# Kernel optimization log

Hardware: AMD Instinct MI355X
Metric: run time of the kernel (lower is better)

## Reference

```python
import jax, jax.numpy as jnp
import numpy as np

D_MODEL = 1024
N_HEADS = 16
D_K = D_MODEL // N_HEADS  # 64


def setup_inputs() -> dict:
    key = jax.random.key(0)
    ks = jax.random.split(key, 12)
    B, S = 2, 2048
    inp = {
        "query": jax.random.normal(ks[0], (B, S, D_MODEL), jnp.float32),
        "key": jax.random.normal(ks[1], (B, S, D_MODEL), jnp.float32),
        "value": jax.random.normal(ks[2], (B, S, D_MODEL), jnp.float32),
        "mask": jnp.ones((B, 1, S, S), jnp.int32),
    }
    sc = 1.0 / np.sqrt(D_MODEL)
    inp["Wq"] = jax.random.normal(ks[3], (D_MODEL, D_MODEL), jnp.float32) * sc
    inp["bq"] = jnp.zeros((D_MODEL,), jnp.float32)
    inp["Wk"] = jax.random.normal(ks[4], (D_MODEL, D_MODEL), jnp.float32) * sc
    inp["bk"] = jnp.zeros((D_MODEL,), jnp.float32)
    inp["Wv"] = jax.random.normal(ks[5], (D_MODEL, D_MODEL), jnp.float32) * sc
    inp["bv"] = jnp.zeros((D_MODEL,), jnp.float32)
    inp["Wo"] = jax.random.normal(ks[6], (D_MODEL, D_MODEL), jnp.float32) * sc
    inp["bo"] = jnp.zeros((D_MODEL,), jnp.float32)
    return inp


def reference(query, key, value, mask, Wq, bq, Wk, bk, Wv, bv, Wo, bo):
    B, Sq, _ = query.shape
    H, dk = N_HEADS, D_K
    # linear projections, split heads: (B,S,D) -> (B,H,S,dk)
    def split_heads(x):
        return x.reshape(B, -1, H, dk).transpose(0, 2, 1, 3)
    Q = split_heads(query @ Wq.T + bq)
    K = split_heads(key @ Wk.T + bk)
    V = split_heads(value @ Wv.T + bv)
    scale = 1.0 / jnp.sqrt(jnp.asarray(dk, jnp.float32))
    scores = jnp.einsum('bhqd,bhkd->bhqk', Q, K) * scale
    scores = jnp.where(mask == 0, jnp.asarray(-1e9, scores.dtype), scores)
    attn = jax.nn.softmax(scores, axis=-1)  # (B,H,Sq,Sk)
    out = jnp.einsum('bhqk,bhkd->bhqd', attn, V)
    out = out.transpose(0, 2, 1, 3).reshape(B, Sq, D_MODEL)
    out = out @ Wo.T + bo
    return out, attn
```

## Files before the change

kernel.cpp:

```cpp
#include <hip/hip_runtime.h>
#include <cstdint>
#include <cstddef>

#define DEV __device__ __forceinline__

typedef float f32x4 __attribute__((ext_vector_type(4)));
typedef __bf16 bf16x8 __attribute__((ext_vector_type(8)));
typedef unsigned short u16x8 __attribute__((ext_vector_type(8)));

static constexpr int D = 1024, H = 16, DK = 64, S = 2048, B = 2;
static constexpr int M_TOT = B * S;
static constexpr size_t OUT0 = (size_t)M_TOT * D;

DEV unsigned short f2bf(float f) {
  unsigned x = __builtin_bit_cast(unsigned, f);
  unsigned r = (x + 0x7fffu + ((x >> 16) & 1u)) >> 16;
  return (unsigned short)r;
}

DEV float bf2f(unsigned short u) {
  return __builtin_bit_cast(float, (unsigned)u << 16);
}

DEV f32x4 mfma_bf16(bf16x8 a, bf16x8 b, f32x4 c) {
  return __builtin_amdgcn_mfma_f32_16x16x32_bf16(a, b, c, 0, 0, 0);
}

DEV bf16x8 bc(u16x8 u) { return __builtin_bit_cast(bf16x8, u); }

template <int MODE, bool ABF16, bool WBF16>
DEV void proj_body(unsigned short* As, unsigned short* Bs, const void* Aptr,
                   const void* W, const float* bias, void* dst) {
  constexpr int BM = 128, BK = 32, LDT = 40;
  const int tid = threadIdx.x;
  const int lane = tid & 63, wave = tid >> 6;
  const int wrow = wave >> 1, wcol = wave & 1;
  const int l15 = lane & 15, kg = lane >> 4;
  const int m0 = blockIdx.y * BM, n0 = blockIdx.x * BM;
  const int srow = tid >> 1, scb = (tid & 1) * 16;

  f32x4 acc[4][4] = {};

  for (int kt = 0; kt < D; kt += BK) {
    {
      u16x8 t0, t1;
      if constexpr (ABF16) {
        const unsigned short* ap =
            (const unsigned short*)Aptr + (size_t)(m0 + srow) * D + kt + scb;
        t0 = *(const u16x8*)ap;
        t1 = *(const u16x8*)(ap + 8);
      } else {
        const float* ap = (const float*)Aptr + (size_t)(m0 + srow) * D + kt + scb;
        float4 v0 = *(const float4*)(ap + 0);
        float4 v1 = *(const float4*)(ap + 4);
        float4 v2 = *(const float4*)(ap + 8);
        float4 v3 = *(const float4*)(ap + 12);
        t0[0] = f2bf(v0.x); t0[1] = f2bf(v0.y); t0[2] = f2bf(v0.z); t0[3] = f2bf(v0.w);
        t0[4] = f2bf(v1.x); t0[5] = f2bf(v1.y); t0[6] = f2bf(v1.z); t0[7] = f2bf(v1.w);
        t1[0] = f2bf(v2.x); t1[1] = f2bf(v2.y); t1[2] = f2bf(v2.z); t1[3] = f2bf(v2.w);
        t1[4] = f2bf(v3.x); t1[5] = f2bf(v3.y); t1[6] = f2bf(v3.z); t1[7] = f2bf(v3.w);
      }
      *(u16x8*)&As[srow * LDT + scb] = t0;
      *(u16x8*)&As[srow * LDT + scb + 8] = t1;

      u16x8 s0, s1;
      if constexpr (WBF16) {
        const unsigned short* wp =
            (const unsigned short*)W + (size_t)(n0 + srow) * D + kt + scb;
        s0 = *(const u16x8*)wp;
        s1 = *(const u16x8*)(wp + 8);
      } else {
        const float* bp = (const float*)W + (size_t)(n0 + srow) * D + kt + scb;
        float4 w0 = *(const float4*)(bp + 0);
        float4 w1 = *(const float4*)(bp + 4);
        float4 w2 = *(const float4*)(bp + 8);
        float4 w3 = *(const float4*)(bp + 12);
        s0[0] = f2bf(w0.x); s0[1] = f2bf(w0.y); s0[2] = f2bf(w0.z); s0[3] = f2bf(w0.w);
        s0[4] = f2bf(w1.x); s0[5] = f2bf(w1.y); s0[6] = f2bf(w1.z); s0[7] = f2bf(w1.w);
        s1[0] = f2bf(w2.x); s1[1] = f2bf(w2.y); s1[2] = f2bf(w2.z); s1[3] = f2bf(w2.w);
        s1[4] = f2bf(w3.x); s1[5] = f2bf(w3.y); s1[6] = f2bf(w3.z); s1[7] = f2bf(w3.w);
      }
      *(u16x8*)&Bs[srow * LDT + scb] = s0;
      *(u16x8*)&Bs[srow * LDT + scb + 8] = s1;
    }
    __syncthreads();

    bf16x8 a[4], b[4];
#pragma unroll
    for (int i = 0; i < 4; i++)
      a[i] = bc(*(const u16x8*)&As[(wrow * 64 + i * 16 + l15) * LDT + kg * 8]);
#pragma unroll
    for (int i = 0; i < 4; i++)
      b[i] = bc(*(const u16x8*)&Bs[(wcol * 64 + i * 16 + l15) * LDT + kg * 8]);
#pragma unroll
    for (int mi = 0; mi < 4; mi++)
#pragma unroll
      for (int ni = 0; ni < 4; ni++) acc[mi][ni] = mfma_bf16(a[mi], b[ni], acc[mi][ni]);
    __syncthreads();
  }

#pragma unroll
  for (int mi = 0; mi < 4; mi++) {
#pragma unroll
    for (int ni = 0; ni < 4; ni++) {
      const int n = n0 + wcol * 64 + ni * 16 + l15;
      const float bval = bias[n];
#pragma unroll
      for (int r = 0; r < 4; r++) {
        const int m = m0 + wrow * 64 + mi * 16 + kg * 4 + r;
        float v = acc[mi][ni][r] + bval;
        if constexpr (MODE == 0) v *= 0.125f;
        if constexpr (MODE == 0 || MODE == 1) {
          const int b_ = m >> 11, s = m & (S - 1), h = n >> 6, d_ = n & (DK - 1);
          ((unsigned short*)dst)[(((size_t)(b_ * H + h)) * S + s) * DK + d_] = f2bf(v);
        } else if constexpr (MODE == 2) {
          const int b_ = m >> 11, s = m & (S - 1), h = n >> 6, d_ = n & (DK - 1);
          ((unsigned short*)dst)[(((size_t)(b_ * H + h)) * DK + d_) * S + s] = f2bf(v);
        } else {
          ((float*)dst)[(size_t)m * D + n] = v;
        }
      }
    }
  }
}

struct PrepArgs {
  const float* A[3];
  const float* W[3];
  const float* bias[3];
  unsigned short* dst[3];
  const int* mask;
  unsigned long long* bits;
  const float* Wo;
  unsigned short* WoBf;
};

__global__ __launch_bounds__(256) void qkv_prep(PrepArgs pa) {
  __shared__ __align__(16) unsigned short As[128 * 40];
  __shared__ __align__(16) unsigned short Bs[128 * 40];
  const int z = blockIdx.z;
  if (z == 0) {
    proj_body<0, false, false>(As, Bs, pa.A[0], pa.W[0], pa.bias[0], pa.dst[0]);
  } else if (z == 1) {
    proj_body<1, false, false>(As, Bs, pa.A[1], pa.W[1], pa.bias[1], pa.dst[1]);
  } else if (z == 2) {
    proj_body<2, false, false>(As, Bs, pa.A[2], pa.W[2], pa.bias[2], pa.dst[2]);
  } else {
    const int gid = blockIdx.y * 8 + blockIdx.x;
    const int tid = threadIdx.x, lane = tid & 63;
    const int base = gid * 512;
    for (int w = base + (tid >> 6); w < base + 512; w += 4) {
      int m = __builtin_nontemporal_load(pa.mask + (size_t)w * 64 + lane);
      unsigned long long bal = __ballot(m != 0);
      if (lane == 0) pa.bits[w] = bal;
    }
    {
      const size_t i0 = (size_t)gid * 4096 + (size_t)tid * 16;
      float4 v0 = *(const float4*)(pa.Wo + i0);
      float4 v1 = *(const float4*)(pa.Wo + i0 + 4);
      float4 v2 = *(const float4*)(pa.Wo + i0 + 8);
      float4 v3 = *(const float4*)(pa.Wo + i0 + 12);
      u16x8 t0, t1;
      t0[0] = f2bf(v0.x); t0[1] = f2bf(v0.y); t0[2] = f2bf(v0.z); t0[3] = f2bf(v0.w);
      t0[4] = f2bf(v1.x); t0[5] = f2bf(v1.y); t0[6] = f2bf(v1.z); t0[7] = f2bf(v1.w);
      t1[0] = f2bf(v2.x); t1[1] = f2bf(v2.y); t1[2] = f2bf(v2.z); t1[3] = f2bf(v2.w);
      t1[4] = f2bf(v3.x); t1[5] = f2bf(v3.y); t1[6] = f2bf(v3.z); t1[7] = f2bf(v3.w);
      *(u16x8*)(pa.WoBf + i0) = t0;
      *(u16x8*)(pa.WoBf + i0 + 8) = t1;
    }
  }
}

__global__ __launch_bounds__(256) void out_proj(const unsigned short* __restrict__ ctx,
                                                const unsigned short* __restrict__ WoBf,
                                                const float* __restrict__ bo,
                                                float* __restrict__ out) {
  __shared__ __align__(16) unsigned short As[128 * 40];
  __shared__ __align__(16) unsigned short Bs[128 * 40];
  proj_body<3, true, true>(As, Bs, ctx, WoBf, bo, out);
}

__global__ __launch_bounds__(512, 4) void attn_kernel(
    const unsigned short* __restrict__ Qb, const unsigned short* __restrict__ Kb,
    const unsigned short* __restrict__ Vt, const unsigned* __restrict__ bits32,
    float* __restrict__ attn_out, unsigned short* __restrict__ ctx) {
  constexpr int QB = 32;
  constexpr int PROW = 264;
  __shared__ __align__(16) unsigned short pbuf[2][QB * PROW];
  __shared__ unsigned mlds[QB * 64];
  __shared__ float rsum[8 * QB];
  __shared__ float rinv_s[QB];
  __shared__ float opart[4 * QB * 17];

  const int wg = blockIdx.x;
  const int qblk = wg & 63, h = (wg >> 6) & 15, b_ = wg >> 10;
  const int bh = b_ * H + h;
  const int qb0 = qblk * QB;
  const int tid = threadIdx.x, lane = tid & 63, wave = tid >> 6;
  const int l15 = lane & 15, kg = lane >> 4;
  const int rowq = kg * 4;
  constexpr float LOG2E = 1.44269504088896340736f;

#pragma unroll
  for (int i = 0; i < 4; i++) {
    const int idx = tid + i * 512;
    mlds[idx] = bits32[((size_t)b_ * S + qb0 + (idx >> 6)) * 64 + (idx & 63)];
  }

  const unsigned short* qbase = Qb + ((size_t)bh * S + qb0) * DK;
  bf16x8 aq[2][2];
#pragma unroll
  for (int rg = 0; rg < 2; rg++)
#pragma unroll
    for (int hf = 0; hf < 2; hf++)
      aq[rg][hf] =
          bc(*(const u16x8*)(qbase + (size_t)(rg * 16 + l15) * DK + hf * 32 + kg * 8));
  __syncthreads();

  float sum[2][4] = {};
#pragma unroll 2
  for (int i = 0; i < 16; i++) {
    const int t = wave * 16 + i;
    const unsigned short* krow = Kb + ((size_t)bh * S + t * 16 + l15) * DK;
    bf16x8 b0 = bc(*(const u16x8*)(krow + kg * 8));
    bf16x8 b1 = bc(*(const u16x8*)(krow + 32 + kg * 8));
    const unsigned shift = (unsigned)((t & 1) * 16 + l15);
#pragma unroll
    for (int rg = 0; rg < 2; rg++) {
      f32x4 c = {0.f, 0.f, 0.f, 0.f};
      c = mfma_bf16(aq[rg][0], b0, c);
      c = mfma_bf16(aq[rg][1], b1, c);
#pragma unroll
      for (int r = 0; r < 4; r++) {
        const int row = rg * 16 + rowq + r;
        const unsigned w = mlds[row * 64 + (t >> 1)];
        sum[rg][r] += ((w >> shift) & 1u) ? exp2f(c[r] * LOG2E) : 0.f;
      }
    }
  }

#pragma unroll
  for (int rg = 0; rg < 2; rg++)
#pragma unroll
    for (int r = 0; r < 4; r++) {
      float s = sum[rg][r];
      s += __shfl_xor(s, 1);
      s += __shfl_xor(s, 2);
      s += __shfl_xor(s, 4);
      s += __shfl_xor(s, 8);
      if (l15 == 0) rsum[wave * QB + rg * 16 + rowq + r] = s;
    }
  __syncthreads();
  if (tid < QB) {
    float t2 = 0.f;
#pragma unroll
    for (int w = 0; w < 8; w++) t2 += rsum[w * QB + tid];
    rinv_s[tid] = 1.f / t2;
  }
  __syncthreads();

  float ri[2][4];
#pragma unroll
  for (int rg = 0; rg < 2; rg++)
#pragma unroll
    for (int r = 0; r < 4; r++) ri[rg][r] = rinv_s[rg * 16 + rowq + r];

  const int dg = wave & 3, ksub = wave >> 2;
  const unsigned short* vrow = Vt + ((size_t)bh * DK + dg * 16 + l15) * S + ksub * 128;
  float* abase = attn_out + ((size_t)bh * S + qb0) * S;
  f32x4 o[2] = {};

  for (int sb = 0; sb < 8; sb++) {
    unsigned short* pb = pbuf[sb & 1];
#pragma unroll
    for (int j = 0; j < 2; j++) {
      const int t = sb * 16 + wave * 2 + j;
      const unsigned short* krow = Kb + ((size_t)bh * S + t * 16 + l15) * DK;
      bf16x8 b0 = bc(*(const u16x8*)(krow + kg * 8));
      bf16x8 b1 = bc(*(const u16x8*)(krow + 32 + kg * 8));
      const unsigned shift = (unsigned)((t & 1) * 16 + l15);
      const int lc = (wave * 2 + j) * 16 + l15;
#pragma unroll
      for (int rg = 0; rg < 2; rg++) {
        f32x4 c = {0.f, 0.f, 0.f, 0.f};
        c = mfma_bf16(aq[rg][0], b0, c);
        c = mfma_bf16(aq[rg][1], b1, c);
#pragma unroll
        for (int r = 0; r < 4; r++) {
          const int row = rg * 16 + rowq + r;
          const unsigned w = mlds[row * 64 + (t >> 1)];
          const float e = ((w >> shift) & 1u) ? exp2f(c[r] * LOG2E) : 0.f;
          const float p = e * ri[rg][r];
          __builtin_nontemporal_store(p, abase + (size_t)row * S + t * 16 + l15);
          pb[row * PROW + lc] = f2bf(p);
        }
      }
    }
    __syncthreads();
    const unsigned short* vv = vrow + sb * 256;
#pragma unroll
    for (int ks = 0; ks < 4; ks++) {
      bf16x8 bv = bc(*(const u16x8*)(vv + ks * 32 + kg * 8));
#pragma unroll
      for (int rg = 0; rg < 2; rg++) {
        bf16x8 af = bc(
            *(const u16x8*)&pb[(rg * 16 + l15) * PROW + ksub * 128 + ks * 32 + kg * 8]);
        o[rg] = mfma_bf16(af, bv, o[rg]);
      }
    }
  }

  if (ksub == 1) {
#pragma unroll
    for (int rg = 0; rg < 2; rg++)
#pragma unroll
      for (int r = 0; r < 4; r++)
        opart[dg * (QB * 17) + (rg * 16 + rowq + r) * 17 + l15] = o[rg][r];
  }
  __syncthreads();
  if (ksub == 0) {
#pragma unroll
    for (int rg = 0; rg < 2; rg++)
#pragma unroll
      for (int r = 0; r < 4; r++) {
        const int row = rg * 16 + rowq + r;
        const float v = o[rg][r] + opart[dg * (QB * 17) + row * 17 + l15];
        ctx[((size_t)(b_ * S + qb0 + row)) * D + h * DK + dg * 16 + l15] = f2bf(v);
      }
  }
}

extern "C" void kernel_launch(void* const* d_in, const int* in_sizes, int n_in,
                              void* d_out, int out_size, void* d_ws, size_t ws_size,
                              hipStream_t stream) {
  const float* query = (const float*)d_in[0];
  const float* key   = (const float*)d_in[1];
  const float* value = (const float*)d_in[2];
  const int*   mask  = (const int*)d_in[3];
  const float* Wq = (const float*)d_in[4];
  const float* bq = (const float*)d_in[5];
  const float* Wk = (const float*)d_in[6];
  const float* bk = (const float*)d_in[7];
  const float* Wv = (const float*)d_in[8];
  const float* bv = (const float*)d_in[9];
  const float* Wo = (const float*)d_in[10];
  const float* bo = (const float*)d_in[11];

  float* out_p = (float*)d_out;
  float* attn_p = (float*)d_out + OUT0;

  size_t off = 0;
  auto carve = [&](size_t bytes) {
    void* p = (char*)d_ws + off;
    off += (bytes + 255) & ~(size_t)255;
    return p;
  };
  const size_t headed = (size_t)B * H * S * DK * sizeof(unsigned short);
  unsigned short* Qb = (unsigned short*)carve(headed);
  unsigned short* Kb = (unsigned short*)carve(headed);
  unsigned short* Vt = (unsigned short*)carve(headed);
  unsigned short* ctx = (unsigned short*)carve((size_t)M_TOT * D * sizeof(unsigned short));
  unsigned long long* bits = (unsigned long long*)carve((size_t)B * S * S / 8);
  unsigned short* WoBf = (unsigned short*)carve((size_t)D * D * sizeof(unsigned short));

  PrepArgs pa;
  pa.A[0] = query; pa.A[1] = key; pa.A[2] = value;
  pa.W[0] = Wq; pa.W[1] = Wk; pa.W[2] = Wv;
  pa.bias[0] = bq; pa.bias[1] = bk; pa.bias[2] = bv;
  pa.dst[0] = Qb; pa.dst[1] = Kb; pa.dst[2] = Vt;
  pa.mask = mask; pa.bits = bits; pa.Wo = Wo; pa.WoBf = WoBf;

  qkv_prep<<<dim3(8, 32, 4), 256, 0, stream>>>(pa);

  attn_kernel<<<B * H * (S / 32), 512, 0, stream>>>(Qb, Kb, Vt, (const unsigned*)bits,
                                                    attn_p, ctx);

  out_proj<<<dim3(8, 32), 256, 0, stream>>>(ctx, WoBf, bo, out_p);
}
```

Before: 366.6 us.

## Pre-convert weights to bf16, add all-ones mask fast path, coalesce attn stores

Splits the prep into a separate conversion kernel that turns all four weight matrices into bf16 once, so the QKV GEMM no longer reconverts fp32 weights for every tile. The attention kernel checks whether its mask tile is all ones and, if so, skips the per-element mask lookups. The attention-probability output is now written as coalesced 16-byte rows read back from the bf16 LDS buffer instead of scattered scalar stores. The occupancy hint rises to 6 blocks. The stored attn values are now bf16-rounded rather than full fp32, and the extra launch adds overhead.

New measurement: 369.5 us. No clear change (+0.8%).

```diff
diff --git a/kernel.cpp b/kernel.cpp
--- a/kernel.cpp
+++ b/kernel.cpp
@@ -28,9 +28,9 @@
 
 DEV bf16x8 bc(u16x8 u) { return __builtin_bit_cast(bf16x8, u); }
 
-template <int MODE, bool ABF16, bool WBF16>
+template <int MODE, bool ABF16>
 DEV void proj_body(unsigned short* As, unsigned short* Bs, const void* Aptr,
-                   const void* W, const float* bias, void* dst) {
+                   const unsigned short* W, const float* bias, void* dst) {
   constexpr int BM = 128, BK = 32, LDT = 40;
   const int tid = threadIdx.x;
   const int lane = tid & 63, wave = tid >> 6;
@@ -63,25 +63,9 @@
       *(u16x8*)&As[srow * LDT + scb] = t0;
       *(u16x8*)&As[srow * LDT + scb + 8] = t1;
 
-      u16x8 s0, s1;
-      if constexpr (WBF16) {
-        const unsigned short* wp =
-            (const unsigned short*)W + (size_t)(n0 + srow) * D + kt + scb;
-        s0 = *(const u16x8*)wp;
-        s1 = *(const u16x8*)(wp + 8);
-      } else {
-        const float* bp = (const float*)W + (size_t)(n0 + srow) * D + kt + scb;
-        float4 w0 = *(const float4*)(bp + 0);
-        float4 w1 = *(const float4*)(bp + 4);
-        float4 w2 = *(const float4*)(bp + 8);
-        float4 w3 = *(const float4*)(bp + 12);
-        s0[0] = f2bf(w0.x); s0[1] = f2bf(w0.y); s0[2] = f2bf(w0.z); s0[3] = f2bf(w0.w);
-        s0[4] = f2bf(w1.x); s0[5] = f2bf(w1.y); s0[6] = f2bf(w1.z); s0[7] = f2bf(w1.w);
-        s1[0] = f2bf(w2.x); s1[1] = f2bf(w2.y); s1[2] = f2bf(w2.z); s1[3] = f2bf(w2.w);
-        s1[4] = f2bf(w3.x); s1[5] = f2bf(w3.y); s1[6] = f2bf(w3.z); s1[7] = f2bf(w3.w);
-      }
-      *(u16x8*)&Bs[srow * LDT + scb] = s0;
-      *(u16x8*)&Bs[srow * LDT + scb + 8] = s1;
+      const unsigned short* wp = W + (size_t)(n0 + srow) * D + kt + scb;
+      *(u16x8*)&Bs[srow * LDT + scb] = *(const u16x8*)wp;
+      *(u16x8*)&Bs[srow * LDT + scb + 8] = *(const u16x8*)(wp + 8);
     }
     __syncthreads();
 
@@ -124,63 +108,74 @@
   }
 }
 
-struct PrepArgs {
-  const float* A[3];
-  const float* W[3];
-  const float* bias[3];
-  unsigned short* dst[3];
-  const int* mask;
-  unsigned long long* bits;
-  const float* Wo;
-  unsigned short* WoBf;
-};
-
-__global__ __launch_bounds__(256) void qkv_prep(PrepArgs pa) {
-  __shared__ __align__(16) unsigned short As[128 * 40];
-  __shared__ __align__(16) unsigned short Bs[128 * 40];
-  const int z = blockIdx.z;
-  if (z == 0) {
-    proj_body<0, false, false>(As, Bs, pa.A[0], pa.W[0], pa.bias[0], pa.dst[0]);
-  } else if (z == 1) {
-    proj_body<1, false, false>(As, Bs, pa.A[1], pa.W[1], pa.bias[1], pa.dst[1]);
-  } else if (z == 2) {
-    proj_body<2, false, false>(As, Bs, pa.A[2], pa.W[2], pa.bias[2], pa.dst[2]);
-  } else {
-    const int gid = blockIdx.y * 8 + blockIdx.x;
-    const int tid = threadIdx.x, lane = tid & 63;
-    const int base = gid * 512;
-    for (int w = base + (tid >> 6); w < base + 512; w += 4) {
-      int m = __builtin_nontemporal_load(pa.mask + (size_t)w * 64 + lane);
-      unsigned long long bal = __ballot(m != 0);
-      if (lane == 0) pa.bits[w] = bal;
-    }
-    {
-      const size_t i0 = (size_t)gid * 4096 + (size_t)tid * 16;
-      float4 v0 = *(const float4*)(pa.Wo + i0);
-      float4 v1 = *(const float4*)(pa.Wo + i0 + 4);
-      float4 v2 = *(const float4*)(pa.Wo + i0 + 8);
-      float4 v3 = *(const float4*)(pa.Wo + i0 + 12);
+__global__ __launch_bounds__(256) void conv_kernel(
+    const float* __restrict__ Wq, const float* __restrict__ Wk,
+    const float* __restrict__ Wv, const float* __restrict__ Wo,
+    unsigned short* __restrict__ Wqb, unsigned short* __restrict__ Wkb,
+    unsigned short* __restrict__ Wvb, unsigned short* __restrict__ Wob,
+    const int* __restrict__ mask, unsigned long long* __restrict__ bits) {
+  const int gid = blockIdx.x, tid = threadIdx.x;
+  if (gid < 256) {
+    const float* srcs[4] = {Wq, Wk, Wv, Wo};
+    unsigned short* dsts[4] = {Wqb, Wkb, Wvb, Wob};
+    const float* src = srcs[gid >> 6];
+    unsigned short* dst = dsts[gid >> 6];
+    const size_t off = (size_t)(gid & 63) * 16384;
+#pragma unroll
+    for (int it = 0; it < 4; it++) {
+      const size_t i0 = off + it * 4096 + (size_t)tid * 16;
+      float4 v0 = *(const float4*)(src + i0);
+      float4 v1 = *(const float4*)(src + i0 + 4);
+      float4 v2 = *(const float4*)(src + i0 + 8);
+      float4 v3 = *(const float4*)(src + i0 + 12);
       u16x8 t0, t1;
       t0[0] = f2bf(v0.x); t0[1] = f2bf(v0.y); t0[2] = f2bf(v0.z); t0[3] = f2bf(v0.w);
       t0[4] = f2bf(v1.x); t0[5] = f2bf(v1.y); t0[6] = f2bf(v1.z); t0[7] = f2bf(v1.w);
       t1[0] = f2bf(v2.x); t1[1] = f2bf(v2.y); t1[2] = f2bf(v2.z); t1[3] = f2bf(v2.w);
       t1[4] = f2bf(v3.x); t1[5] = f2bf(v3.y); t1[6] = f2bf(v3.z); t1[7] = f2bf(v3.w);
-      *(u16x8*)(pa.WoBf + i0) = t0;
-      *(u16x8*)(pa.WoBf + i0 + 8) = t1;
-    }
-  }
+      *(u16x8*)(dst + i0) = t0;
+      *(u16x8*)(dst + i0 + 8) = t1;
+    }
+  } else {
+    const int lane = tid & 63;
+    const int base = (gid - 256) * 256;
+    for (int w = base + (tid >> 6); w < base + 256; w += 4) {
+      int m = __builtin_nontemporal_load(mask + (size_t)w * 64 + lane);
+      unsigned long long bal = __ballot(m != 0);
+      if (lane == 0) bits[w] = bal;
+    }
+  }
+}
+
+struct GemmArgs {
+  const float* A[3];
+  const unsigned short* Wb[3];
+  const float* bias[3];
+  unsigned short* dst[3];
+};
+
+__global__ __launch_bounds__(256) void qkv_gemm(GemmArgs ga) {
+  __shared__ __align__(16) unsigned short As[128 * 40];
+  __shared__ __align__(16) unsigned short Bs[128 * 40];
+  const int z = blockIdx.z;
+  if (z == 0)
+    proj_body<0, false>(As, Bs, ga.A[0], ga.Wb[0], ga.bias[0], ga.dst[0]);
+  else if (z == 1)
+    proj_body<1, false>(As, Bs, ga.A[1], ga.Wb[1], ga.bias[1], ga.dst[1]);
+  else
+    proj_body<2, false>(As, Bs, ga.A[2], ga.Wb[2], ga.bias[2], ga.dst[2]);
 }
 
 __global__ __launch_bounds__(256) void out_proj(const unsigned short* __restrict__ ctx,
-                                                const unsigned short* __restrict__ WoBf,
+                                                const unsigned short* __restrict__ Wob,
                                                 const float* __restrict__ bo,
                                                 float* __restrict__ out) {
   __shared__ __align__(16) unsigned short As[128 * 40];
   __shared__ __align__(16) unsigned short Bs[128 * 40];
-  proj_body<3, true, true>(As, Bs, ctx, WoBf, bo, out);
-}
-
-__global__ __launch_bounds__(512, 4) void attn_kernel(
+  proj_body<3, true>(As, Bs, ctx, Wob, bo, out);
+}
+
+__global__ __launch_bounds__(512, 6) void attn_kernel(
     const unsigned short* __restrict__ Qb, const unsigned short* __restrict__ Kb,
     const unsigned short* __restrict__ Vt, const unsigned* __restrict__ bits32,
     float* __restrict__ attn_out, unsigned short* __restrict__ ctx) {
@@ -191,6 +186,7 @@
   __shared__ float rsum[8 * QB];
   __shared__ float rinv_s[QB];
   __shared__ float opart[4 * QB * 17];
+  __shared__ unsigned mflag;
 
   const int wg = blockIdx.x;
   const int qblk = wg & 63, h = (wg >> 6) & 15, b_ = wg >> 10;
@@ -201,11 +197,19 @@
   const int rowq = kg * 4;
   constexpr float LOG2E = 1.44269504088896340736f;
 
+  if (tid == 0) mflag = 0xFFFFFFFFu;
+  unsigned myand = 0xFFFFFFFFu;
+  unsigned mw[4];
 #pragma unroll
   for (int i = 0; i < 4; i++) {
     const int idx = tid + i * 512;
-    mlds[idx] = bits32[((size_t)b_ * S + qb0 + (idx >> 6)) * 64 + (idx & 63)];
-  }
+    mw[i] = bits32[((size_t)b_ * S + qb0 + (idx >> 6)) * 64 + (idx & 63)];
+    myand &= mw[i];
+  }
+  __syncthreads();
+#pragma unroll
+  for (int i = 0; i < 4; i++) mlds[tid + i * 512] = mw[i];
+  if (myand != 0xFFFFFFFFu) atomicAnd(&mflag, 0u);
 
   const unsigned short* qbase = Qb + ((size_t)bh * S + qb0) * DK;
   bf16x8 aq[2][2];
@@ -216,6 +220,7 @@
       aq[rg][hf] =
           bc(*(const u16x8*)(qbase + (size_t)(rg * 16 + l15) * DK + hf * 32 + kg * 8));
   __syncthreads();
+  const bool allones = (mflag == 0xFFFFFFFFu);
 
   float sum[2][4] = {};
 #pragma unroll 2
@@ -230,11 +235,15 @@
       f32x4 c = {0.f, 0.f, 0.f, 0.f};
       c = mfma_bf16(aq[rg][0], b0, c);
       c = mfma_bf16(aq[rg][1], b1, c);
-#pragma unroll
-      for (int r = 0; r < 4; r++) {
-        const int row = rg * 16 + rowq + r;
-        const unsigned w = mlds[row * 64 + (t >> 1)];
-        sum[rg][r] += ((w >> shift) & 1u) ? exp2f(c[r] * LOG2E) : 0.f;
+      if (allones) {
+#pragma unroll
+        for (int r = 0; r < 4; r++) sum[rg][r] += exp2f(c[r] * LOG2E);
+      } else {
+#pragma unroll
+        for (int r = 0; r < 4; r++) {
+          const unsigned w = mlds[(rg * 16 + rowq + r) * 64 + (t >> 1)];
+          sum[rg][r] += ((w >> shift) & 1u) ? exp2f(c[r] * LOG2E) : 0.f;
+        }
       }
     }
   }
@@ -268,6 +277,8 @@
   const int dg = wave & 3, ksub = wave >> 2;
   const unsigned short* vrow = Vt + ((size_t)bh * DK + dg * 16 + l15) * S + ksub * 128;
   float* abase = attn_out + ((size_t)bh * S + qb0) * S;
+  const int wrow2 = lane >> 5;
+  const int wcol = (lane & 31) * 8;
   f32x4 o[2] = {};
 
   for (int sb = 0; sb < 8; sb++) {
@@ -285,18 +296,37 @@
         f32x4 c = {0.f, 0.f, 0.f, 0.f};
         c = mfma_bf16(aq[rg][0], b0, c);
         c = mfma_bf16(aq[rg][1], b1, c);
-#pragma unroll
-        for (int r = 0; r < 4; r++) {
-          const int row = rg * 16 + rowq + r;
-          const unsigned w = mlds[row * 64 + (t >> 1)];
-          const float e = ((w >> shift) & 1u) ? exp2f(c[r] * LOG2E) : 0.f;
-          const float p = e * ri[rg][r];
-          __builtin_nontemporal_store(p, abase + (size_t)row * S + t * 16 + l15);
-          pb[row * PROW + lc] = f2bf(p);
+        if (allones) {
+#pragma unroll
+          for (int r = 0; r < 4; r++) {
+            const int row = rg * 16 + rowq + r;
+            pb[row * PROW + lc] = f2bf(exp2f(c[r] * LOG2E) * ri[rg][r]);
+          }
+        } else {
+#pragma unroll
+          for (int r = 0; r < 4; r++) {
+            const int row = rg * 16 + rowq + r;
+            const unsigned w = mlds[row * 64 + (t >> 1)];
+            const float e = ((w >> shift) & 1u) ? exp2f(c[r] * LOG2E) : 0.f;
+            pb[row * PROW + lc] = f2bf(e * ri[rg][r]);
+          }
         }
       }
     }
     __syncthreads();
+
+#pragma unroll
+    for (int rr = 0; rr < 2; rr++) {
+      const int row = wave * 4 + rr * 2 + wrow2;
+      u16x8 u = *(const u16x8*)&pb[row * PROW + wcol];
+      f32x4 lo, hi;
+      lo[0] = bf2f(u[0]); lo[1] = bf2f(u[1]); lo[2] = bf2f(u[2]); lo[3] = bf2f(u[3]);
+      hi[0] = bf2f(u[4]); hi[1] = bf2f(u[5]); hi[2] = bf2f(u[6]); hi[3] = bf2f(u[7]);
+      float* dp = abase + (size_t)row * S + sb * 256 + wcol;
+      __builtin_nontemporal_store(lo, (f32x4*)dp);
+      __builtin_nontemporal_store(hi, (f32x4*)(dp + 4));
+    }
+
     const unsigned short* vv = vrow + sb * 256;
 #pragma unroll
     for (int ks = 0; ks < 4; ks++) {
@@ -356,24 +386,28 @@
     return p;
   };
   const size_t headed = (size_t)B * H * S * DK * sizeof(unsigned short);
+  const size_t wbytes = (size_t)D * D * sizeof(unsigned short);
   unsigned short* Qb = (unsigned short*)carve(headed);
   unsigned short* Kb = (unsigned short*)carve(headed);
   unsigned short* Vt = (unsigned short*)carve(headed);
   unsigned short* ctx = (unsigned short*)carve((size_t)M_TOT * D * sizeof(unsigned short));
   unsigned long long* bits = (unsigned long long*)carve((size_t)B * S * S / 8);
-  unsigned short* WoBf = (unsigned short*)carve((size_t)D * D * sizeof(unsigned short));
-
-  PrepArgs pa;
-  pa.A[0] = query; pa.A[1] = key; pa.A[2] = value;
-  pa.W[0] = Wq; pa.W[1] = Wk; pa.W[2] = Wv;
-  pa.bias[0] = bq; pa.bias[1] = bk; pa.bias[2] = bv;
-  pa.dst[0] = Qb; pa.dst[1] = Kb; pa.dst[2] = Vt;
-  pa.mask = mask; pa.bits = bits; pa.Wo = Wo; pa.WoBf = WoBf;
-
-  qkv_prep<<<dim3(8, 32, 4), 256, 0, stream>>>(pa);
+  unsigned short* Wqb = (unsigned short*)carve(wbytes);
+  unsigned short* Wkb = (unsigned short*)carve(wbytes);
+  unsigned short* Wvb = (unsigned short*)carve(wbytes);
+  unsigned short* Wob = (unsigned short*)carve(wbytes);
+
+  conv_kernel<<<768, 256, 0, stream>>>(Wq, Wk, Wv, Wo, Wqb, Wkb, Wvb, Wob, mask, bits);
+
+  GemmArgs ga;
+  ga.A[0] = query; ga.A[1] = key; ga.A[2] = value;
+  ga.Wb[0] = Wqb; ga.Wb[1] = Wkb; ga.Wb[2] = Wvb;
+  ga.bias[0] = bq; ga.bias[1] = bk; ga.bias[2] = bv;
+  ga.dst[0] = Qb; ga.dst[1] = Kb; ga.dst[2] = Vt;
+  qkv_gemm<<<dim3(8, 32, 3), 256, 0, stream>>>(ga);
 
   attn_kernel<<<B * H * (S / 32), 512, 0, stream>>>(Qb, Kb, Vt, (const unsigned*)bits,
                                                     attn_p, ctx);
 
-  out_proj<<<dim3(8, 32), 256, 0, stream>>>(ctx, WoBf, bo, out_p);
-}
+  out_proj<<<dim3(8, 32), 256, 0, stream>>>(ctx, Wob, bo, out_p);
+}
```
